# Performance work log

Hardware: AMD Instinct MI355X
Metric: run time of the kernel (lower is better)

The kernel has to match this reference:

```python
import jax, jax.numpy as jnp
import numpy as np

N_NODES = 50000
N_EDGES = 600000
D = 128


def setup_inputs() -> dict:
    key = jax.random.key(0)
    k1, k2, k3, k4 = jax.random.split(key, 4)
    x = jax.random.normal(k1, (N_NODES, D), dtype=jnp.float32)
    edge_index = jax.random.randint(k2, (2, N_EDGES), 0, N_NODES, dtype=jnp.int64)
    # GCNConv linear weight (glorot-ish scale) and bias
    W = jax.random.normal(k3, (D, D), dtype=jnp.float32) * (1.0 / np.sqrt(D))
    b = jax.random.normal(k4, (D,), dtype=jnp.float32) * 0.01
    return {"x": x, "edge_index": edge_index, "W": W, "b": b}


def reference(x, edge_index, W, b):
    """ResGCN: x + GCNConv(x, edge_index).

    GCNConv (PyG defaults): add self-loops, symmetric deg^{-1/2} normalization,
    messages x_j @ W scattered to destination nodes edge_index[1], plus bias.
    """
    n = x.shape[0]
    loop = jnp.arange(n, dtype=edge_index.dtype)
    src = jnp.concatenate([edge_index[0], loop])  # [E+N]
    dst = jnp.concatenate([edge_index[1], loop])  # [E+N]

    # degree on destination nodes (includes self-loops, edge_weight = 1)
    deg = jax.ops.segment_sum(jnp.ones(src.shape[0], x.dtype), dst, num_segments=n)
    deg_inv_sqrt = jnp.where(deg > 0, jax.lax.rsqrt(deg), jnp.zeros_like(deg))
    norm = deg_inv_sqrt[src] * deg_inv_sqrt[dst]  # [E+N]

    xw = x @ W  # [N, D] transform once, gather after
    msg = xw[src] * norm[:, None]  # [E+N, D]
    agg = jax.ops.segment_sum(msg, dst, num_segments=n)  # [N, D]
    res = agg + b
    return x + res
```

## Files before the change

### kernel.cpp

```cpp
#include <hip/hip_runtime.h>
#include <cstdint>

#define DD  128
#define CAP 32
#define SEB 2048
#define OVC 1024

typedef __attribute__((ext_vector_type(8))) short bf16x8;
typedef __attribute__((ext_vector_type(8))) unsigned short ushort8_t;
typedef __attribute__((ext_vector_type(4))) float f32x4;
typedef __attribute__((ext_vector_type(2))) float f32x2;

__device__ __forceinline__ short f2bf(float f) {
    union { float f; unsigned u; } v; v.f = f;
    unsigned r = v.u + 0x7FFFu + ((v.u >> 16) & 1u);
    return (short)(r >> 16);
}
__device__ __forceinline__ float bf2f(unsigned short s) {
    union { unsigned u; float f; } v; v.u = ((unsigned)s) << 16;
    return v.f;
}
__device__ __forceinline__ int load_idx(const void* ei, int flag, long long pos) {
    if (flag) return ((const int*)ei)[pos];
    return (int)((const long long*)ei)[pos];
}

__global__ __launch_bounds__(256) void stage_gemm(const void* ei, int E, int N,
                                                  int SBLK,
                                                  unsigned* __restrict__ seg,
                                                  int* __restrict__ blkhist,
                                                  int* __restrict__ blkoff,
                                                  const float* __restrict__ W,
                                                  const float* __restrict__ x,
                                                  short* __restrict__ xw,
                                                  unsigned char* __restrict__ xwq) {
    union SMem {
        struct {
            unsigned epack[SEB];
            unsigned sorted[SEB];
            int hist[256];
            int scan[256];
            int curs[256];
            int flag;
        } st;
        short wp[DD * 136];
    };
    __shared__ SMem sm;
    const int tid = threadIdx.x;
    const int bid = blockIdx.x;

    if (bid < SBLK) {
        if (tid == 0) sm.st.flag = 0;
        __syncthreads();
        {
            const int n = E < 256 ? E : 256;
            if (tid < n) {
                const long long v = ((const long long*)ei)[tid];
                if (v < 0 || v >= (1LL << 32)) atomicOr(&sm.st.flag, 1);
            }
        }
        __syncthreads();
        const int f = sm.st.flag;
        const int base_e = bid * SEB;
        const int ne = min(SEB, E - base_e);

        for (int i = tid; i < ne; i += 256) {
            const unsigned s = (unsigned)load_idx(ei, f, base_e + i);
            const unsigned t = (unsigned)load_idx(ei, f, (long long)E + base_e + i);
            sm.st.epack[i] = (t << 16) | s;
        }
        sm.st.hist[tid] = 0;
        __syncthreads();
        for (int i = tid; i < ne; i += 256)
            atomicAdd(&sm.st.hist[sm.st.epack[i] >> 24], 1);
        __syncthreads();
        const int hval = sm.st.hist[tid];
        blkhist[bid * 256 + tid] = hval;
        sm.st.scan[tid] = hval;
        __syncthreads();
        for (int off = 1; off < 256; off <<= 1) {
            const int v = (tid >= off) ? sm.st.scan[tid - off] : 0;
            __syncthreads();
            sm.st.scan[tid] += v;
            __syncthreads();
        }
        const int boff = sm.st.scan[tid] - hval;
        blkoff[bid * 256 + tid] = boff;
        sm.st.curs[tid] = boff;
        __syncthreads();
        for (int i = tid; i < ne; i += 256) {
            const unsigned u = sm.st.epack[i];
            const int pos = atomicAdd(&sm.st.curs[u >> 24], 1);
            sm.st.sorted[pos] = u & 0x00FFFFFFu;
        }
        __syncthreads();
        for (int i = tid; i < ne; i += 256)
            seg[(size_t)bid * SEB + i] = sm.st.sorted[i];
        return;
    }

    for (int e = tid; e < DD * DD; e += 256) {
        const int k = e >> 7, n = e & 127;
        sm.wp[n * 136 + k] = f2bf(W[e]);
    }
    __syncthreads();

    const int tile = bid - SBLK;
    const int wave = tid >> 6;
    const int lane = tid & 63;
    const int lmod = lane & 15;
    const int lgrp = lane >> 4;
    const int rowbase = tile * 64 + wave * 16;
    const int arow = rowbase + lmod;
    const bool aok = arow < N;

    f32x4 acc[8];
#pragma unroll
    for (int i = 0; i < 8; ++i) acc[i] = (f32x4){0.f, 0.f, 0.f, 0.f};

#pragma unroll
    for (int ks = 0; ks < 4; ++ks) {
        const int kbase = ks * 32 + lgrp * 8;
        bf16x8 afrag;
        if (aok) {
            const float4 a0 = *(const float4*)&x[(size_t)arow * DD + kbase];
            const float4 a1 = *(const float4*)&x[(size_t)arow * DD + kbase + 4];
            afrag[0] = f2bf(a0.x); afrag[1] = f2bf(a0.y);
            afrag[2] = f2bf(a0.z); afrag[3] = f2bf(a0.w);
            afrag[4] = f2bf(a1.x); afrag[5] = f2bf(a1.y);
            afrag[6] = f2bf(a1.z); afrag[7] = f2bf(a1.w);
        } else {
#pragma unroll
            for (int i = 0; i < 8; ++i) afrag[i] = 0;
        }
#pragma unroll
        for (int nt = 0; nt < 8; ++nt) {
            const bf16x8 bfrag = *(const bf16x8*)&sm.wp[(nt * 16 + lmod) * 136 + kbase];
            acc[nt] = __builtin_amdgcn_mfma_f32_16x16x32_bf16(afrag, bfrag, acc[nt], 0, 0, 0);
        }
    }

#pragma unroll
    for (int r = 0; r < 4; ++r) {
        const int row = rowbase + lgrp * 4 + r;
        if (row < N) {
#pragma unroll
            for (int nt = 0; nt < 8; ++nt) {
                const float v = acc[nt][r];
                xw[(size_t)row * DD + nt * 16 + lmod] = f2bf(v);
                const unsigned q = __builtin_amdgcn_cvt_pk_fp8_f32(v, v, 0, false);
                xwq[(size_t)row * DD + nt * 16 + lmod] = (unsigned char)(q & 0xFF);
            }
        }
    }
}

__global__ __launch_bounds__(256) void bucket_kernel(const unsigned* __restrict__ seg,
                                                     const int* __restrict__ blkhist,
                                                     const int* __restrict__ blkoff,
                                                     int SBLK, int N,
                                                     unsigned* __restrict__ ovArea,
                                                     int* __restrict__ ovcnt,
                                                     int* __restrict__ col,
                                                     int* __restrict__ cnt) {
    const int part = blockIdx.x;
    const int node0 = part << 8;
    __shared__ int lcnt[256];
    __shared__ int lov;
    lcnt[threadIdx.x] = 0;
    if (threadIdx.x == 0) lov = 0;
    __syncthreads();

    for (int b = threadIdx.x; b < SBLK; b += 256) {
        const int off = blkoff[b * 256 + part];
        const int h   = blkhist[b * 256 + part];
        const unsigned* s = &seg[(size_t)b * SEB + off];
        for (int k = 0; k < h; ++k) {
            const unsigned u = s[k];
            const int dstl = (u >> 16) & 0xFF;
            const int r = atomicAdd(&lcnt[dstl], 1);
            if (r < CAP) col[(node0 + dstl) * CAP + r] = (int)(u & 0xFFFFu);
            else {
                const int o = atomicAdd(&lov, 1);
                if (o < OVC) ovArea[part * OVC + o] = u;
            }
        }
    }
    __syncthreads();
    const int node = node0 + threadIdx.x;
    if (node < N) cnt[node] = lcnt[threadIdx.x];
    if (threadIdx.x == 0) ovcnt[part] = lov;
}

__global__ __launch_bounds__(256) void gather_kernel(const short* __restrict__ xw,
                                                     const unsigned char* __restrict__ xwq,
                                                     const float* __restrict__ x,
                                                     const float* __restrict__ b,
                                                     const int* __restrict__ cnt,
                                                     const int* __restrict__ col,
                                                     const unsigned* __restrict__ ovArea,
                                                     const int* __restrict__ ovcnt,
                                                     const unsigned* __restrict__ seg,
                                                     const int* __restrict__ blkhist,
                                                     const int* __restrict__ blkoff,
                                                     int SBLK,
                                                     float* __restrict__ out, int N) {
    const int node = blockIdx.x * 16 + (threadIdx.x >> 4);
    if (node >= N) return;
    const int l = threadIdx.x & 15;
    const ushort8_t* xw8 = (const ushort8_t*)xw;
    const uint2* xq2 = (const uint2*)xwq;

    const int deg = cnt[node];
    const int nbk = deg < CAP ? deg : CAP;
    const float d = rsqrtf((float)(deg + 1));

    const float4 x0 = *(const float4*)&x[(size_t)node * DD + l * 8];
    const float4 x1 = *(const float4*)&x[(size_t)node * DD + l * 8 + 4];
    const float4 b0 = *(const float4*)&b[l * 8];
    const float4 b1 = *(const float4*)&b[l * 8 + 4];

    const int2 ir = ((const int2*)col)[node * 16 + l];
    const int s0 = (2 * l     < nbk) ? ir.x : 0;
    const int s1 = (2 * l + 1 < nbk) ? ir.y : 0;
    const float dsa = rsqrtf((float)(cnt[s0] + 1));
    const float dsb = rsqrtf((float)(cnt[s1] + 1));

    float acc[8], ac2[8];
    const ushort8_t sv = xw8[(size_t)node * 16 + l];
#pragma unroll
    for (int e = 0; e < 8; ++e) { acc[e] = d * bf2f(sv[e]); ac2[e] = 0.f; }

    int j = 0;
    for (; j + 8 <= nbk; j += 8) {
        int   sj[8];
        float dj[8];
#pragma unroll
        for (int u = 0; u < 8; ++u) {
            sj[u] = __shfl((u & 1) ? s1 : s0, (j + u) >> 1, 16);
            dj[u] = __shfl((u & 1) ? dsb : dsa, (j + u) >> 1, 16);
        }
        uint2 v[8];
#pragma unroll
        for (int u = 0; u < 8; ++u) v[u] = xq2[(size_t)sj[u] * 16 + l];
#pragma unroll
        for (int u = 0; u < 8; ++u) {
            float* A = (u & 1) ? ac2 : acc;
            const f32x2 p0 = __builtin_amdgcn_cvt_pk_f32_fp8(v[u].x, false);
            const f32x2 p1 = __builtin_amdgcn_cvt_pk_f32_fp8(v[u].x, true);
            const f32x2 p2 = __builtin_amdgcn_cvt_pk_f32_fp8(v[u].y, false);
            const f32x2 p3 = __builtin_amdgcn_cvt_pk_f32_fp8(v[u].y, true);
            A[0] = fmaf(dj[u], p0[0], A[0]); A[1] = fmaf(dj[u], p0[1], A[1]);
            A[2] = fmaf(dj[u], p1[0], A[2]); A[3] = fmaf(dj[u], p1[1], A[3]);
            A[4] = fmaf(dj[u], p2[0], A[4]); A[5] = fmaf(dj[u], p2[1], A[5]);
            A[6] = fmaf(dj[u], p3[0], A[6]); A[7] = fmaf(dj[u], p3[1], A[7]);
        }
    }
    for (; j + 4 <= nbk; j += 4) {
        int   sj[4];
        float dj[4];
#pragma unroll
        for (int u = 0; u < 4; ++u) {
            sj[u] = __shfl((u & 1) ? s1 : s0, (j + u) >> 1, 16);
            dj[u] = __shfl((u & 1) ? dsb : dsa, (j + u) >> 1, 16);
        }
        uint2 v[4];
#pragma unroll
        for (int u = 0; u < 4; ++u) v[u] = xq2[(size_t)sj[u] * 16 + l];
#pragma unroll
        for (int u = 0; u < 4; ++u) {
            float* A = (u & 1) ? ac2 : acc;
            const f32x2 p0 = __builtin_amdgcn_cvt_pk_f32_fp8(v[u].x, false);
            const f32x2 p1 = __builtin_amdgcn_cvt_pk_f32_fp8(v[u].x, true);
            const f32x2 p2 = __builtin_amdgcn_cvt_pk_f32_fp8(v[u].y, false);
            const f32x2 p3 = __builtin_amdgcn_cvt_pk_f32_fp8(v[u].y, true);
            A[0] = fmaf(dj[u], p0[0], A[0]); A[1] = fmaf(dj[u], p0[1], A[1]);
            A[2] = fmaf(dj[u], p1[0], A[2]); A[3] = fmaf(dj[u], p1[1], A[3]);
            A[4] = fmaf(dj[u], p2[0], A[4]); A[5] = fmaf(dj[u], p2[1], A[5]);
            A[6] = fmaf(dj[u], p3[0], A[6]); A[7] = fmaf(dj[u], p3[1], A[7]);
        }
    }
    for (; j < nbk; ++j) {
        const int   sj = __shfl((j & 1) ? s1 : s0, j >> 1, 16);
        const float dj = __shfl((j & 1) ? dsb : dsa, j >> 1, 16);
        const uint2 v = xq2[(size_t)sj * 16 + l];
        const f32x2 p0 = __builtin_amdgcn_cvt_pk_f32_fp8(v.x, false);
        const f32x2 p1 = __builtin_amdgcn_cvt_pk_f32_fp8(v.x, true);
        const f32x2 p2 = __builtin_amdgcn_cvt_pk_f32_fp8(v.y, false);
        const f32x2 p3 = __builtin_amdgcn_cvt_pk_f32_fp8(v.y, true);
        acc[0] = fmaf(dj, p0[0], acc[0]); acc[1] = fmaf(dj, p0[1], acc[1]);
        acc[2] = fmaf(dj, p1[0], acc[2]); acc[3] = fmaf(dj, p1[1], acc[3]);
        acc[4] = fmaf(dj, p2[0], acc[4]); acc[5] = fmaf(dj, p2[1], acc[5]);
        acc[6] = fmaf(dj, p3[0], acc[6]); acc[7] = fmaf(dj, p3[1], acc[7]);
    }

    if (deg > CAP) {
        const int part = node >> 8, dl = node & 255;
        const int oc = ovcnt[part];
        if (oc <= OVC) {
            for (int i = 0; i < oc; ++i) {
                const unsigned u = ovArea[part * OVC + i];
                if ((int)((u >> 16) & 0xFF) == dl) {
                    const int src = (int)(u & 0xFFFFu);
                    const float dss = rsqrtf((float)(cnt[src] + 1));
                    const ushort8_t v = xw8[(size_t)src * 16 + l];
#pragma unroll
                    for (int e = 0; e < 8; ++e) acc[e] = fmaf(dss, bf2f(v[e]), acc[e]);
                }
            }
        } else {
#pragma unroll
            for (int e = 0; e < 8; ++e) { acc[e] = d * bf2f(sv[e]); ac2[e] = 0.f; }
            for (int bb = 0; bb < SBLK; ++bb) {
                const int off = blkoff[bb * 256 + part];
                const int h   = blkhist[bb * 256 + part];
                for (int k = 0; k < h; ++k) {
                    const unsigned u = seg[(size_t)bb * SEB + off + k];
                    if ((int)((u >> 16) & 0xFF) == dl) {
                        const int src = (int)(u & 0xFFFFu);
                        const float dss = rsqrtf((float)(cnt[src] + 1));
                        const ushort8_t v = xw8[(size_t)src * 16 + l];
#pragma unroll
                        for (int e = 0; e < 8; ++e) acc[e] = fmaf(dss, bf2f(v[e]), acc[e]);
                    }
                }
            }
        }
    }

    float4 o0, o1;
    o0.x = x0.x + b0.x + d * (acc[0] + ac2[0]);
    o0.y = x0.y + b0.y + d * (acc[1] + ac2[1]);
    o0.z = x0.z + b0.z + d * (acc[2] + ac2[2]);
    o0.w = x0.w + b0.w + d * (acc[3] + ac2[3]);
    o1.x = x1.x + b1.x + d * (acc[4] + ac2[4]);
    o1.y = x1.y + b1.y + d * (acc[5] + ac2[5]);
    o1.z = x1.z + b1.z + d * (acc[6] + ac2[6]);
    o1.w = x1.w + b1.w + d * (acc[7] + ac2[7]);
    *(float4*)&out[(size_t)node * DD + l * 8]     = o0;
    *(float4*)&out[(size_t)node * DD + l * 8 + 4] = o1;
}

extern "C" void kernel_launch(void* const* d_in, const int* in_sizes, int n_in,
                              void* d_out, int out_size, void* d_ws, size_t ws_size,
                              hipStream_t stream) {
    const float* x  = (const float*)d_in[0];
    const void*  ei = d_in[1];
    const float* W  = (const float*)d_in[2];
    const float* b  = (const float*)d_in[3];
    float* out = (float*)d_out;

    const int N = in_sizes[0] / DD;
    const int E = in_sizes[1] / 2;

    const int SBLK  = (E + SEB - 1) / SEB;
    const int npart = (N + 255) >> 8;

    char* ws = (char*)d_ws;
    size_t off = 0;
    unsigned* seg = (unsigned*)(ws + off);      off += (size_t)SBLK * SEB * 4;
    int* blkhist  = (int*)(ws + off);           off += (size_t)SBLK * 256 * 4;
    int* blkoff   = (int*)(ws + off);           off += (size_t)SBLK * 256 * 4;
    int* cnt      = (int*)(ws + off);           off += (size_t)N * 4;
    int* col      = (int*)(ws + off);           off += (size_t)N * CAP * 4;
    int* ovcnt    = (int*)(ws + off);           off += 256 * 4;
    unsigned* ovArea = (unsigned*)(ws + off);   off += (size_t)npart * OVC * 4;
    off = (off + 255) & ~(size_t)255;
    short* xw = (short*)(ws + off);             off += (size_t)N * DD * 2;
    unsigned char* xwq = (unsigned char*)(ws + off);

    const int GB = (N + 63) / 64;
    stage_gemm<<<SBLK + GB, 256, 0, stream>>>(ei, E, N, SBLK, seg, blkhist, blkoff,
                                              W, x, xw, xwq);
    bucket_kernel<<<npart, 256, 0, stream>>>(seg, blkhist, blkoff, SBLK, N,
                                             ovArea, ovcnt, col, cnt);
    gather_kernel<<<(N + 15) / 16, 256, 0, stream>>>(xw, xwq, x, b, cnt, col,
                                                     ovArea, ovcnt, seg, blkhist,
                                                     blkoff, SBLK, out, N);
}
```

Before: 67.66 us.

## Halve GEMM blocks, store 16-bit column indices, precompute per-node inverse sqrt degree

Each GEMM block now handles 128 rows in two passes, so the bf16 conversion of W into shared memory is paid over twice as many rows and the GEMM grid is halved. The CSR-like column array shrinks from int to unsigned short, halving its write and read traffic. The bucket kernel now writes a per-node deg^{-1/2} array, so the gather kernel loads one float per neighbour instead of loading a count and computing rsqrt. The trade-off is less GEMM parallelism and an extra N-float buffer.

```diff
diff --git a/kernel.cpp b/kernel.cpp
--- a/kernel.cpp
+++ b/kernel.cpp
@@ -110,46 +110,50 @@
     const int lane = tid & 63;
     const int lmod = lane & 15;
     const int lgrp = lane >> 4;
-    const int rowbase = tile * 64 + wave * 16;
-    const int arow = rowbase + lmod;
-    const bool aok = arow < N;
-
-    f32x4 acc[8];
-#pragma unroll
-    for (int i = 0; i < 8; ++i) acc[i] = (f32x4){0.f, 0.f, 0.f, 0.f};
-
-#pragma unroll
-    for (int ks = 0; ks < 4; ++ks) {
-        const int kbase = ks * 32 + lgrp * 8;
-        bf16x8 afrag;
-        if (aok) {
-            const float4 a0 = *(const float4*)&x[(size_t)arow * DD + kbase];
-            const float4 a1 = *(const float4*)&x[(size_t)arow * DD + kbase + 4];
-            afrag[0] = f2bf(a0.x); afrag[1] = f2bf(a0.y);
-            afrag[2] = f2bf(a0.z); afrag[3] = f2bf(a0.w);
-            afrag[4] = f2bf(a1.x); afrag[5] = f2bf(a1.y);
-            afrag[6] = f2bf(a1.z); afrag[7] = f2bf(a1.w);
-        } else {
-#pragma unroll
-            for (int i = 0; i < 8; ++i) afrag[i] = 0;
-        }
-#pragma unroll
-        for (int nt = 0; nt < 8; ++nt) {
-            const bf16x8 bfrag = *(const bf16x8*)&sm.wp[(nt * 16 + lmod) * 136 + kbase];
-            acc[nt] = __builtin_amdgcn_mfma_f32_16x16x32_bf16(afrag, bfrag, acc[nt], 0, 0, 0);
-        }
-    }
-
-#pragma unroll
-    for (int r = 0; r < 4; ++r) {
-        const int row = rowbase + lgrp * 4 + r;
-        if (row < N) {
+
+    for (int half = 0; half < 2; ++half) {
+        const int rowbase = tile * 128 + half * 64 + wave * 16;
+        const int arow = rowbase + lmod;
+        const bool aok = arow < N;
+        if (rowbase >= N) break;
+
+        f32x4 acc[8];
+#pragma unroll
+        for (int i = 0; i < 8; ++i) acc[i] = (f32x4){0.f, 0.f, 0.f, 0.f};
+
+#pragma unroll
+        for (int ks = 0; ks < 4; ++ks) {
+            const int kbase = ks * 32 + lgrp * 8;
+            bf16x8 afrag;
+            if (aok) {
+                const float4 a0 = *(const float4*)&x[(size_t)arow * DD + kbase];
+                const float4 a1 = *(const float4*)&x[(size_t)arow * DD + kbase + 4];
+                afrag[0] = f2bf(a0.x); afrag[1] = f2bf(a0.y);
+                afrag[2] = f2bf(a0.z); afrag[3] = f2bf(a0.w);
+                afrag[4] = f2bf(a1.x); afrag[5] = f2bf(a1.y);
+                afrag[6] = f2bf(a1.z); afrag[7] = f2bf(a1.w);
+            } else {
+#pragma unroll
+                for (int i = 0; i < 8; ++i) afrag[i] = 0;
+            }
 #pragma unroll
             for (int nt = 0; nt < 8; ++nt) {
-                const float v = acc[nt][r];
-                xw[(size_t)row * DD + nt * 16 + lmod] = f2bf(v);
-                const unsigned q = __builtin_amdgcn_cvt_pk_fp8_f32(v, v, 0, false);
-                xwq[(size_t)row * DD + nt * 16 + lmod] = (unsigned char)(q & 0xFF);
+                const bf16x8 bfrag = *(const bf16x8*)&sm.wp[(nt * 16 + lmod) * 136 + kbase];
+                acc[nt] = __builtin_amdgcn_mfma_f32_16x16x32_bf16(afrag, bfrag, acc[nt], 0, 0, 0);
+            }
+        }
+
+#pragma unroll
+        for (int r = 0; r < 4; ++r) {
+            const int row = rowbase + lgrp * 4 + r;
+            if (row < N) {
+#pragma unroll
+                for (int nt = 0; nt < 8; ++nt) {
+                    const float v = acc[nt][r];
+                    xw[(size_t)row * DD + nt * 16 + lmod] = f2bf(v);
+                    const unsigned q = __builtin_amdgcn_cvt_pk_fp8_f32(v, v, 0, false);
+                    xwq[(size_t)row * DD + nt * 16 + lmod] = (unsigned char)(q & 0xFF);
+                }
             }
         }
     }
@@ -161,8 +165,9 @@
                                                      int SBLK, int N,
                                                      unsigned* __restrict__ ovArea,
                                                      int* __restrict__ ovcnt,
-                                                     int* __restrict__ col,
-                                                     int* __restrict__ cnt) {
+                                                     unsigned short* __restrict__ col,
+                                                     int* __restrict__ cnt,
+                                                     float* __restrict__ dis) {
     const int part = blockIdx.x;
     const int node0 = part << 8;
     __shared__ int lcnt[256];
@@ -179,7 +184,7 @@
             const unsigned u = s[k];
             const int dstl = (u >> 16) & 0xFF;
             const int r = atomicAdd(&lcnt[dstl], 1);
-            if (r < CAP) col[(node0 + dstl) * CAP + r] = (int)(u & 0xFFFFu);
+            if (r < CAP) col[(size_t)(node0 + dstl) * CAP + r] = (unsigned short)(u & 0xFFFFu);
             else {
                 const int o = atomicAdd(&lov, 1);
                 if (o < OVC) ovArea[part * OVC + o] = u;
@@ -188,7 +193,11 @@
     }
     __syncthreads();
     const int node = node0 + threadIdx.x;
-    if (node < N) cnt[node] = lcnt[threadIdx.x];
+    if (node < N) {
+        const int c = lcnt[threadIdx.x];
+        cnt[node] = c;
+        dis[node] = rsqrtf((float)(c + 1));
+    }
     if (threadIdx.x == 0) ovcnt[part] = lov;
 }
 
@@ -197,7 +206,8 @@
                                                      const float* __restrict__ x,
                                                      const float* __restrict__ b,
                                                      const int* __restrict__ cnt,
-                                                     const int* __restrict__ col,
+                                                     const float* __restrict__ dis,
+                                                     const unsigned short* __restrict__ col,
                                                      const unsigned* __restrict__ ovArea,
                                                      const int* __restrict__ ovcnt,
                                                      const unsigned* __restrict__ seg,
@@ -220,11 +230,11 @@
     const float4 b0 = *(const float4*)&b[l * 8];
     const float4 b1 = *(const float4*)&b[l * 8 + 4];
 
-    const int2 ir = ((const int2*)col)[node * 16 + l];
-    const int s0 = (2 * l     < nbk) ? ir.x : 0;
-    const int s1 = (2 * l + 1 < nbk) ? ir.y : 0;
-    const float dsa = rsqrtf((float)(cnt[s0] + 1));
-    const float dsb = rsqrtf((float)(cnt[s1] + 1));
+    const unsigned ir = ((const unsigned*)col)[(size_t)node * 16 + l];
+    const int s0 = (2 * l     < nbk) ? (int)(ir & 0xFFFFu) : 0;
+    const int s1 = (2 * l + 1 < nbk) ? (int)(ir >> 16) : 0;
+    const float dsa = dis[s0];
+    const float dsb = dis[s1];
 
     float acc[8], ac2[8];
     const ushort8_t sv = xw8[(size_t)node * 16 + l];
@@ -302,10 +312,9 @@
                 const unsigned u = ovArea[part * OVC + i];
                 if ((int)((u >> 16) & 0xFF) == dl) {
                     const int src = (int)(u & 0xFFFFu);
-                    const float dss = rsqrtf((float)(cnt[src] + 1));
                     const ushort8_t v = xw8[(size_t)src * 16 + l];
 #pragma unroll
-                    for (int e = 0; e < 8; ++e) acc[e] = fmaf(dss, bf2f(v[e]), acc[e]);
+                    for (int e = 0; e < 8; ++e) acc[e] = fmaf(dis[src], bf2f(v[e]), acc[e]);
                 }
             }
         } else {
@@ -318,10 +327,9 @@
                     const unsigned u = seg[(size_t)bb * SEB + off + k];
                     if ((int)((u >> 16) & 0xFF) == dl) {
                         const int src = (int)(u & 0xFFFFu);
-                        const float dss = rsqrtf((float)(cnt[src] + 1));
                         const ushort8_t v = xw8[(size_t)src * 16 + l];
 #pragma unroll
-                        for (int e = 0; e < 8; ++e) acc[e] = fmaf(dss, bf2f(v[e]), acc[e]);
+                        for (int e = 0; e < 8; ++e) acc[e] = fmaf(dis[src], bf2f(v[e]), acc[e]);
                     }
                 }
             }
@@ -362,19 +370,21 @@
     int* blkhist  = (int*)(ws + off);           off += (size_t)SBLK * 256 * 4;
     int* blkoff   = (int*)(ws + off);           off += (size_t)SBLK * 256 * 4;
     int* cnt      = (int*)(ws + off);           off += (size_t)N * 4;
-    int* col      = (int*)(ws + off);           off += (size_t)N * CAP * 4;
+    float* dis    = (float*)(ws + off);         off += (size_t)N * 4;
+    unsigned short* col = (unsigned short*)(ws + off);  off += (size_t)N * CAP * 2;
+    off = (off + 255) & ~(size_t)255;
     int* ovcnt    = (int*)(ws + off);           off += 256 * 4;
     unsigned* ovArea = (unsigned*)(ws + off);   off += (size_t)npart * OVC * 4;
     off = (off + 255) & ~(size_t)255;
     short* xw = (short*)(ws + off);             off += (size_t)N * DD * 2;
     unsigned char* xwq = (unsigned char*)(ws + off);
 
-    const int GB = (N + 63) / 64;
+    const int GB = (N + 127) / 128;
     stage_gemm<<<SBLK + GB, 256, 0, stream>>>(ei, E, N, SBLK, seg, blkhist, blkoff,
                                               W, x, xw, xwq);
     bucket_kernel<<<npart, 256, 0, stream>>>(seg, blkhist, blkoff, SBLK, N,
-                                             ovArea, ovcnt, col, cnt);
-    gather_kernel<<<(N + 15) / 16, 256, 0, stream>>>(xw, xwq, x, b, cnt, col,
+                                             ovArea, ovcnt, col, cnt, dis);
+    gather_kernel<<<(N + 15) / 16, 256, 0, stream>>>(xw, xwq, x, b, cnt, dis, col,
                                                      ovArea, ovcnt, seg, blkhist,
                                                      blkoff, SBLK, out, N);
 }
```

Measured after the change: 62.40 us. -7.8%, faster.
